# Performance work log

Hardware: AMD Instinct MI355X
Metric: run time of the kernel (lower is better)

The kernel has to match this reference:

```python
import jax, jax.numpy as jnp
import numpy as np

K_NN = 16  # number of nearest neighbors (module init arg k)


def setup_inputs() -> dict:
    key = jax.random.key(0)
    k1, k2 = jax.random.split(key)
    xyz = jax.random.normal(k1, (8, 16384, 3), dtype=jnp.float32)
    centers = jax.random.normal(k2, (8, 1024, 3), dtype=jnp.float32)
    return {"xyz": xyz, "centers": centers}


def reference(xyz, centers):
    # avoiding the (B, N, K, 3) broadcast intermediate of the original while
    # computing the same torch.norm(xyz - centers, dim=-1) math.
    x_sq = jnp.sum(xyz * xyz, axis=-1)          # (B, N)
    c_sq = jnp.sum(centers * centers, axis=-1)  # (B, K)
    cross = jnp.einsum('bnd,bkd->bnk', xyz, centers)  # (B, N, K)
    d2 = x_sq[:, :, None] + c_sq[None if False else slice(None), None, :] - 2.0 * cross
    dist = jnp.sqrt(jnp.maximum(d2, 0.0))       # (B, N, K)
    # torch.topk(dist, k, dim=1, largest=False, sorted=True):
    # smallest-k over the N (points) axis, per center.
    neg = -jnp.transpose(dist, (0, 2, 1))       # (B, K, N)
    _, idx = jax.lax.top_k(neg, K_NN)           # (B, K, k), ascending distance
    return jnp.transpose(idx, (0, 2, 1))        # (B, k, K) to match torch dim=1 topk
```

## Files before the change

kernel.cpp:

```cpp
#include <hip/hip_runtime.h>
#include <stdint.h>

#define BB    8
#define NN    16384
#define KK    1024
#define KNN   16
#define QTR   (NN / 4)
#define QGRP  (QTR / 4)
#define NG64  256
#define GCAP  48
#define SCAP  192

typedef unsigned long long u64;
typedef float f32x2 __attribute__((ext_vector_type(2)));

__device__ __forceinline__ f32x2 pk_fma(f32x2 a, f32x2 b, f32x2 c) {
    f32x2 d;
    asm("v_pk_fma_f32 %0, %1, %2, %3" : "=v"(d) : "v"(a), "v"(b), "v"(c));
    return d;
}
__device__ __forceinline__ f32x2 pk_mul(f32x2 a, f32x2 b) {
    f32x2 d;
    asm("v_pk_mul_f32 %0, %1, %2" : "=v"(d) : "v"(a), "v"(b));
    return d;
}
__device__ __forceinline__ f32x2 pk_add(f32x2 a, f32x2 b) {
    f32x2 d;
    asm("v_pk_add_f32 %0, %1, %2" : "=v"(d) : "v"(a), "v"(b));
    return d;
}
__device__ __forceinline__ float min3f(float a, float b, float c) {
    float d;
    asm("v_min3_f32 %0, %1, %2, %3" : "=v"(d) : "v"(a), "v"(b), "v"(c));
    return d;
}

__device__ __forceinline__ u64 shfl_xor_u64(u64 v, int mask) {
    int lo = (int)(uint32_t)v;
    int hi = (int)(uint32_t)(v >> 32);
    lo = __shfl_xor(lo, mask, 64);
    hi = __shfl_xor(hi, mask, 64);
    return ((u64)(uint32_t)hi << 32) | (u64)(uint32_t)lo;
}

__device__ __forceinline__ u64 shfl_u64(u64 v, int src) {
    int lo = __shfl((int)(uint32_t)v, src, 64);
    int hi = __shfl((int)(uint32_t)(v >> 32), src, 64);
    return ((u64)(uint32_t)hi << 32) | (u64)(uint32_t)lo;
}

__device__ __forceinline__ u64 wave_min_u64(u64 v) {
#pragma unroll
    for (int off = 32; off > 0; off >>= 1) {
        u64 o = shfl_xor_u64(v, off);
        v = o < v ? o : v;
    }
    return v;
}

__device__ __forceinline__ void sort64_kv(u64& key, uint32_t& pay, int lane) {
#pragma unroll
    for (int k = 2; k <= 64; k <<= 1) {
#pragma unroll
        for (int j = k >> 1; j > 0; j >>= 1) {
            u64 okey = shfl_xor_u64(key, j);
            uint32_t opay = (uint32_t)__shfl_xor((int)pay, j, 64);
            bool tmin = ((lane & j) == 0) == ((lane & k) == 0);
            bool osm = okey < key;
            bool take = tmin ? osm : !osm;
            if (take) { key = okey; pay = opay; }
        }
    }
}

__device__ __forceinline__ void sort64_k(u64& key, int lane) {
#pragma unroll
    for (int k = 2; k <= 64; k <<= 1) {
#pragma unroll
        for (int j = k >> 1; j > 0; j >>= 1) {
            u64 okey = shfl_xor_u64(key, j);
            bool tmin = ((lane & j) == 0) == ((lane & k) == 0);
            bool osm = okey < key;
            bool take = tmin ? osm : !osm;
            if (take) key = okey;
        }
    }
}

__device__ __forceinline__ float point_d2(const float* xb, int i,
                                          float c0, float c1, float c2, float csq) {
#pragma clang fp contract(off)
    float x0 = xb[i * 3 + 0];
    float x1 = xb[i * 3 + 1];
    float x2 = xb[i * 3 + 2];
    float xsq = (x0 * x0 + x1 * x1) + x2 * x2;
    float cross = __fmaf_rn(x2, c2, __fmaf_rn(x1, c1, x0 * c0));
    float d2 = (xsq + csq) - 2.0f * cross;
    return d2 < 0.0f ? 0.0f : d2;
}

__device__ __attribute__((noinline)) int fallback_scan(const float* xb,
                                                       float c0, float c1, float c2,
                                                       float csq, int lane) {
    u64 list[KNN];
#pragma unroll
    for (int j = 0; j < KNN; ++j) list[j] = ~0ull;
    for (int i = lane; i < NN; i += 64) {
        float d2 = point_d2(xb, i, c0, c1, c2, csq);
        float dist = __fsqrt_rn(d2);
        u64 key = ((u64)__float_as_uint(dist) << 32) | (u64)(uint32_t)i;
        if (key < list[KNN - 1]) {
#pragma unroll
            for (int j = 0; j < KNN; ++j) {
                bool lt = key < list[j];
                u64 lo = lt ? key : list[j];
                u64 hi = lt ? list[j] : key;
                list[j] = lo;
                key = hi;
            }
        }
    }
    int res = 0;
    for (int it = 0; it < KNN; ++it) {
        u64 best = wave_min_u64(list[0]);
        if (it == lane) res = (int)(uint32_t)best;
        if (list[0] == best) {
#pragma unroll
            for (int j = 0; j < KNN - 1; ++j) list[j] = list[j + 1];
            list[KNN - 1] = ~0ull;
        }
    }
    return res;
}

__device__ __forceinline__ float sixteenth_smallest_f(float v, int lane) {
#pragma unroll
    for (int k = 2; k <= 64; k <<= 1) {
#pragma unroll
        for (int j = k >> 1; j > 0; j >>= 1) {
            float o = __shfl_xor(v, j, 64);
            bool takeMin = ((lane & j) == 0) == ((lane & k) == 0);
            float mn = fminf(v, o);
            float mx = fmaxf(v, o);
            v = takeMin ? mn : mx;
        }
    }
    return __shfl(v, 15, 64);
}

__device__ __forceinline__ void repack_pairs(float4 f0, float4 f1, float4 f2,
                                             f32x2& xl, f32x2& xh,
                                             f32x2& yl, f32x2& yh,
                                             f32x2& zl, f32x2& zh,
                                             f32x2& sl, f32x2& sh) {
    xl = f32x2{f0.x, f0.w};  yl = f32x2{f0.y, f1.x};  zl = f32x2{f0.z, f1.y};
    xh = f32x2{f1.z, f2.y};  yh = f32x2{f1.w, f2.z};  zh = f32x2{f2.x, f2.w};
    sl = pk_add(pk_add(pk_mul(xl, xl), pk_mul(yl, yl)), pk_mul(zl, zl));
    sh = pk_add(pk_add(pk_mul(xh, xh), pk_mul(yh, yh)), pk_mul(zh, zh));
}

__global__ __launch_bounds__(256, 8) void knn_kernel(const float* __restrict__ xyz,
                                                     const float* __restrict__ centers,
                                                     int* __restrict__ out) {
#pragma clang fp contract(off)
    const int q = (int)(threadIdx.x >> 6);
    const int lane = (int)(threadIdx.x & 63);
    const int cbase = (int)blockIdx.x * 4;
    const int b = cbase >> 10;

    __shared__ float    s_min[4][NG64];
    __shared__ uint32_t s_glist[4][GCAP];
    __shared__ uint32_t s_idx[4][SCAP];

    f32x2 nx[4], ny[4], nz[4];
#pragma unroll
    for (int c = 0; c < 4; ++c) {
        float a0 = -2.0f * centers[(cbase + c) * 3 + 0];
        float a1 = -2.0f * centers[(cbase + c) * 3 + 1];
        float a2 = -2.0f * centers[(cbase + c) * 3 + 2];
        nx[c] = f32x2{a0, a0};
        ny[c] = f32x2{a1, a1};
        nz[c] = f32x2{a2, a2};
    }

    const float* xb = xyz + (size_t)b * NN * 3;
    const float4* x4 = (const float4*)xb;
    const int gbase = q * QGRP;

    float acc[4];
#pragma unroll
    for (int c = 0; c < 4; ++c) acc[c] = __builtin_inff();
    {
        const float4* p = x4 + (size_t)(gbase + lane) * 3;
#pragma unroll 4
        for (int s = 0; s < QGRP / 64; ++s, p += 192) {
            float4 f0 = p[0], f1 = p[1], f2 = p[2];
            f32x2 xl, xh, yl, yh, zl, zh, sl, sh;
            repack_pairs(f0, f1, f2, xl, xh, yl, yh, zl, zh, sl, sh);
#pragma unroll
            for (int c = 0; c < 4; ++c) {
                f32x2 dl = pk_fma(xl, nx[c], pk_fma(yl, ny[c], pk_fma(zl, nz[c], sl)));
                f32x2 dh = pk_fma(xh, nx[c], pk_fma(yh, ny[c], pk_fma(zh, nz[c], sh)));
                acc[c] = min3f(acc[c], dl.x, dl.y);
                acc[c] = min3f(acc[c], dh.x, dh.y);
            }
        }
    }
#pragma unroll
    for (int c = 0; c < 4; ++c) s_min[c][threadIdx.x] = acc[c];
    __syncthreads();

    float v = fminf(min3f(s_min[q][lane], s_min[q][64 + lane], s_min[q][128 + lane]),
                    s_min[q][192 + lane]);
    float t16 = sixteenth_smallest_f(v, lane);
    const float Uq = t16 + fabsf(t16) * 1e-5f + 5e-4f;
    const u64 ltmask = (1ull << lane) - 1ull;

    int ng = 0;
#pragma unroll
    for (int it = 0; it < NG64 / 64; ++it) {
        int gi = it * 64 + lane;
        bool cnd = s_min[q][gi] <= Uq;
        u64 m = __ballot(cnd);
        int pos = ng + (int)__popcll(m & ltmask);
        if (cnd && pos < GCAP) s_glist[q][pos] = (uint32_t)gi;
        ng += (int)__popcll(m);
    }
    bool ok = (ng <= GCAP);

    int total = 0;
    if (ok) {
        const int tasks = ng * 16;
        const int trips = (tasks + 63) >> 6;
        for (int t = 0; t < trips; ++t) {
            int j = t * 64 + lane;
            bool valid = j < tasks;
            int grp = (int)s_glist[q][valid ? (j >> 4) : 0];
            int ss = j & 15;
            int lg = (grp >> 6) * QGRP + ss * 64 + (grp & 63);
            float4 f0 = x4[lg * 3 + 0];
            float4 f1 = x4[lg * 3 + 1];
            float4 f2 = x4[lg * 3 + 2];
            f32x2 xl, xh, yl, yh, zl, zh, sl, sh;
            repack_pairs(f0, f1, f2, xl, xh, yl, yh, zl, zh, sl, sh);
            f32x2 dl = pk_fma(xl, nx[q], pk_fma(yl, ny[q], pk_fma(zl, nz[q], sl)));
            f32x2 dh = pk_fma(xh, nx[q], pk_fma(yh, ny[q], pk_fma(zh, nz[q], sh)));
            int ibase = lg * 4;
            bool c0v = valid && (dl.x <= Uq);
            bool c1v = valid && (dl.y <= Uq);
            bool c2v = valid && (dh.x <= Uq);
            bool c3v = valid && (dh.y <= Uq);
            u64 m0 = __ballot(c0v), m1 = __ballot(c1v);
            u64 m2 = __ballot(c2v), m3 = __ballot(c3v);
            int p0 = total + (int)__popcll(m0 & ltmask);
            int b1 = total + (int)__popcll(m0);
            int p1 = b1 + (int)__popcll(m1 & ltmask);
            int b2 = b1 + (int)__popcll(m1);
            int p2 = b2 + (int)__popcll(m2 & ltmask);
            int b3 = b2 + (int)__popcll(m2);
            int p3 = b3 + (int)__popcll(m3 & ltmask);
            if (c0v && p0 < SCAP) s_idx[q][p0] = (uint32_t)(ibase + 0);
            if (c1v && p1 < SCAP) s_idx[q][p1] = (uint32_t)(ibase + 1);
            if (c2v && p2 < SCAP) s_idx[q][p2] = (uint32_t)(ibase + 2);
            if (c3v && p3 < SCAP) s_idx[q][p3] = (uint32_t)(ibase + 3);
            total = b3 + (int)__popcll(m3);
        }
        ok = (total <= SCAP);
    }

    const int cc = cbase + q;
    const float c0 = centers[cc * 3 + 0];
    const float c1 = centers[cc * 3 + 1];
    const float c2 = centers[cc * 3 + 2];
    const float csq = (c0 * c0 + c1 * c1) + c2 * c2;

    uint32_t res;
    if (ok) {
        u64 l0 = ~0ull, l1 = ~0ull, l2 = ~0ull, l3 = ~0ull;
        for (int j = lane; j < total; j += 64) {
            int idx = (int)s_idx[q][j];
            float d2 = point_d2(xb, idx, c0, c1, c2, csq);
            u64 key = ((u64)__float_as_uint(__fsqrt_rn(d2)) << 32) | (u64)(uint32_t)idx;
            bool tt;
            tt = key < l0; { u64 lo = tt ? key : l0, hi = tt ? l0 : key; l0 = lo; key = hi; }
            tt = key < l1; { u64 lo = tt ? key : l1, hi = tt ? l1 : key; l1 = lo; key = hi; }
            tt = key < l2; { u64 lo = tt ? key : l2, hi = tt ? l2 : key; l2 = lo; key = hi; }
            tt = key < l3; { u64 lo = tt ? key : l3, hi = tt ? l3 : key; l3 = lo; key = hi; }
        }
        if (total <= 64) {
            sort64_k(l0, lane);
            res = (uint32_t)l0;
        } else {
            u64 key = l0;
            uint32_t pay = (uint32_t)lane;
            sort64_kv(key, pay, lane);
            int pos = lane >> 2, elem = lane & 3;
            int sid = __shfl((int)pay, pos, 64);
            u64 g0 = shfl_u64(l0, sid);
            u64 g1 = shfl_u64(l1, sid);
            u64 g2 = shfl_u64(l2, sid);
            u64 g3 = shfl_u64(l3, sid);
            u64 gk = (elem == 0) ? g0 : (elem == 1) ? g1 : (elem == 2) ? g2 : g3;
            sort64_k(gk, lane);
            res = (uint32_t)gk;
        }
    } else {
        res = (uint32_t)fallback_scan(xb, c0, c1, c2, csq, lane);
    }

    if (lane < KNN) {
        out[((size_t)b * KNN + lane) * KK + (cc & 1023)] = (int)res;
    }
}

extern "C" void kernel_launch(void* const* d_in, const int* in_sizes, int n_in,
                              void* d_out, int out_size, void* d_ws, size_t ws_size,
                              hipStream_t stream) {
    const float* xyz = (const float*)d_in[0];
    const float* centers = (const float*)d_in[1];
    int* out = (int*)d_out;
    (void)d_ws; (void)ws_size;

    const int nblocks = BB * KK / 4;
    hipLaunchKernelGGL(knn_kernel, dim3(nblocks), dim3(256), 0, stream,
                       xyz, centers, out);
}
```

Measured before the change: 91.16 us.

## Process eight centers per block to reuse each streamed point across more centers

```diff
diff --git a/kernel.cpp b/kernel.cpp
--- a/kernel.cpp
+++ b/kernel.cpp
@@ -5,6 +5,7 @@
 #define NN    16384
 #define KK    1024
 #define KNN   16
+#define CPB   8
 #define QTR   (NN / 4)
 #define QGRP  (QTR / 4)
 #define NG64  256
@@ -159,22 +160,22 @@
     sh = pk_add(pk_add(pk_mul(xh, xh), pk_mul(yh, yh)), pk_mul(zh, zh));
 }
 
-__global__ __launch_bounds__(256, 8) void knn_kernel(const float* __restrict__ xyz,
+__global__ __launch_bounds__(256, 4) void knn_kernel(const float* __restrict__ xyz,
                                                      const float* __restrict__ centers,
                                                      int* __restrict__ out) {
 #pragma clang fp contract(off)
     const int q = (int)(threadIdx.x >> 6);
     const int lane = (int)(threadIdx.x & 63);
-    const int cbase = (int)blockIdx.x * 4;
+    const int cbase = (int)blockIdx.x * CPB;
     const int b = cbase >> 10;
 
-    __shared__ float    s_min[4][NG64];
-    __shared__ uint32_t s_glist[4][GCAP];
-    __shared__ uint32_t s_idx[4][SCAP];
-
-    f32x2 nx[4], ny[4], nz[4];
-#pragma unroll
-    for (int c = 0; c < 4; ++c) {
+    __shared__ float    s_min[CPB][NG64];
+    __shared__ uint32_t s_glist[CPB][GCAP];
+    __shared__ uint32_t s_idx[CPB][SCAP];
+
+    f32x2 nx[CPB], ny[CPB], nz[CPB];
+#pragma unroll
+    for (int c = 0; c < CPB; ++c) {
         float a0 = -2.0f * centers[(cbase + c) * 3 + 0];
         float a1 = -2.0f * centers[(cbase + c) * 3 + 1];
         float a2 = -2.0f * centers[(cbase + c) * 3 + 2];
@@ -187,18 +188,18 @@
     const float4* x4 = (const float4*)xb;
     const int gbase = q * QGRP;
 
-    float acc[4];
-#pragma unroll
-    for (int c = 0; c < 4; ++c) acc[c] = __builtin_inff();
+    float acc[CPB];
+#pragma unroll
+    for (int c = 0; c < CPB; ++c) acc[c] = __builtin_inff();
     {
         const float4* p = x4 + (size_t)(gbase + lane) * 3;
-#pragma unroll 4
+#pragma unroll 2
         for (int s = 0; s < QGRP / 64; ++s, p += 192) {
             float4 f0 = p[0], f1 = p[1], f2 = p[2];
             f32x2 xl, xh, yl, yh, zl, zh, sl, sh;
             repack_pairs(f0, f1, f2, xl, xh, yl, yh, zl, zh, sl, sh);
 #pragma unroll
-            for (int c = 0; c < 4; ++c) {
+            for (int c = 0; c < CPB; ++c) {
                 f32x2 dl = pk_fma(xl, nx[c], pk_fma(yl, ny[c], pk_fma(zl, nz[c], sl)));
                 f32x2 dh = pk_fma(xh, nx[c], pk_fma(yh, ny[c], pk_fma(zh, nz[c], sh)));
                 acc[c] = min3f(acc[c], dl.x, dl.y);
@@ -207,109 +208,119 @@
         }
     }
 #pragma unroll
-    for (int c = 0; c < 4; ++c) s_min[c][threadIdx.x] = acc[c];
+    for (int c = 0; c < CPB; ++c) s_min[c][threadIdx.x] = acc[c];
     __syncthreads();
 
-    float v = fminf(min3f(s_min[q][lane], s_min[q][64 + lane], s_min[q][128 + lane]),
-                    s_min[q][192 + lane]);
-    float t16 = sixteenth_smallest_f(v, lane);
-    const float Uq = t16 + fabsf(t16) * 1e-5f + 5e-4f;
     const u64 ltmask = (1ull << lane) - 1ull;
 
-    int ng = 0;
-#pragma unroll
-    for (int it = 0; it < NG64 / 64; ++it) {
-        int gi = it * 64 + lane;
-        bool cnd = s_min[q][gi] <= Uq;
-        u64 m = __ballot(cnd);
-        int pos = ng + (int)__popcll(m & ltmask);
-        if (cnd && pos < GCAP) s_glist[q][pos] = (uint32_t)gi;
-        ng += (int)__popcll(m);
-    }
-    bool ok = (ng <= GCAP);
-
-    int total = 0;
-    if (ok) {
-        const int tasks = ng * 16;
-        const int trips = (tasks + 63) >> 6;
-        for (int t = 0; t < trips; ++t) {
-            int j = t * 64 + lane;
-            bool valid = j < tasks;
-            int grp = (int)s_glist[q][valid ? (j >> 4) : 0];
-            int ss = j & 15;
-            int lg = (grp >> 6) * QGRP + ss * 64 + (grp & 63);
-            float4 f0 = x4[lg * 3 + 0];
-            float4 f1 = x4[lg * 3 + 1];
-            float4 f2 = x4[lg * 3 + 2];
-            f32x2 xl, xh, yl, yh, zl, zh, sl, sh;
-            repack_pairs(f0, f1, f2, xl, xh, yl, yh, zl, zh, sl, sh);
-            f32x2 dl = pk_fma(xl, nx[q], pk_fma(yl, ny[q], pk_fma(zl, nz[q], sl)));
-            f32x2 dh = pk_fma(xh, nx[q], pk_fma(yh, ny[q], pk_fma(zh, nz[q], sh)));
-            int ibase = lg * 4;
-            bool c0v = valid && (dl.x <= Uq);
-            bool c1v = valid && (dl.y <= Uq);
-            bool c2v = valid && (dh.x <= Uq);
-            bool c3v = valid && (dh.y <= Uq);
-            u64 m0 = __ballot(c0v), m1 = __ballot(c1v);
-            u64 m2 = __ballot(c2v), m3 = __ballot(c3v);
-            int p0 = total + (int)__popcll(m0 & ltmask);
-            int b1 = total + (int)__popcll(m0);
-            int p1 = b1 + (int)__popcll(m1 & ltmask);
-            int b2 = b1 + (int)__popcll(m1);
-            int p2 = b2 + (int)__popcll(m2 & ltmask);
-            int b3 = b2 + (int)__popcll(m2);
-            int p3 = b3 + (int)__popcll(m3 & ltmask);
-            if (c0v && p0 < SCAP) s_idx[q][p0] = (uint32_t)(ibase + 0);
-            if (c1v && p1 < SCAP) s_idx[q][p1] = (uint32_t)(ibase + 1);
-            if (c2v && p2 < SCAP) s_idx[q][p2] = (uint32_t)(ibase + 2);
-            if (c3v && p3 < SCAP) s_idx[q][p3] = (uint32_t)(ibase + 3);
-            total = b3 + (int)__popcll(m3);
-        }
-        ok = (total <= SCAP);
-    }
-
-    const int cc = cbase + q;
-    const float c0 = centers[cc * 3 + 0];
-    const float c1 = centers[cc * 3 + 1];
-    const float c2 = centers[cc * 3 + 2];
-    const float csq = (c0 * c0 + c1 * c1) + c2 * c2;
-
-    uint32_t res;
-    if (ok) {
-        u64 l0 = ~0ull, l1 = ~0ull, l2 = ~0ull, l3 = ~0ull;
-        for (int j = lane; j < total; j += 64) {
-            int idx = (int)s_idx[q][j];
-            float d2 = point_d2(xb, idx, c0, c1, c2, csq);
-            u64 key = ((u64)__float_as_uint(__fsqrt_rn(d2)) << 32) | (u64)(uint32_t)idx;
-            bool tt;
-            tt = key < l0; { u64 lo = tt ? key : l0, hi = tt ? l0 : key; l0 = lo; key = hi; }
-            tt = key < l1; { u64 lo = tt ? key : l1, hi = tt ? l1 : key; l1 = lo; key = hi; }
-            tt = key < l2; { u64 lo = tt ? key : l2, hi = tt ? l2 : key; l2 = lo; key = hi; }
-            tt = key < l3; { u64 lo = tt ? key : l3, hi = tt ? l3 : key; l3 = lo; key = hi; }
-        }
-        if (total <= 64) {
-            sort64_k(l0, lane);
-            res = (uint32_t)l0;
+#pragma unroll
+    for (int ci = 0; ci < 2; ++ci) {
+        const int c = q * 2 + ci;
+        const int cc = cbase + c;
+
+        float v = fminf(min3f(s_min[c][lane], s_min[c][64 + lane],
+                              s_min[c][128 + lane]),
+                        s_min[c][192 + lane]);
+        float t16 = sixteenth_smallest_f(v, lane);
+        const float Uq = t16 + fabsf(t16) * 1e-5f + 5e-4f;
+
+        const float a0 = centers[cc * 3 + 0];
+        const float a1 = centers[cc * 3 + 1];
+        const float a2 = centers[cc * 3 + 2];
+        const f32x2 cnx = f32x2{-2.0f * a0, -2.0f * a0};
+        const f32x2 cny = f32x2{-2.0f * a1, -2.0f * a1};
+        const f32x2 cnz = f32x2{-2.0f * a2, -2.0f * a2};
+
+        int ng = 0;
+#pragma unroll
+        for (int it = 0; it < NG64 / 64; ++it) {
+            int gi = it * 64 + lane;
+            bool cnd = s_min[c][gi] <= Uq;
+            u64 m = __ballot(cnd);
+            int pos = ng + (int)__popcll(m & ltmask);
+            if (cnd && pos < GCAP) s_glist[c][pos] = (uint32_t)gi;
+            ng += (int)__popcll(m);
+        }
+        bool ok = (ng <= GCAP);
+
+        int total = 0;
+        if (ok) {
+            const int tasks = ng * 16;
+            const int trips = (tasks + 63) >> 6;
+            for (int t = 0; t < trips; ++t) {
+                int j = t * 64 + lane;
+                bool valid = j < tasks;
+                int grp = (int)s_glist[c][valid ? (j >> 4) : 0];
+                int ss = j & 15;
+                int lg = (grp >> 6) * QGRP + ss * 64 + (grp & 63);
+                float4 f0 = x4[lg * 3 + 0];
+                float4 f1 = x4[lg * 3 + 1];
+                float4 f2 = x4[lg * 3 + 2];
+                f32x2 xl, xh, yl, yh, zl, zh, sl, sh;
+                repack_pairs(f0, f1, f2, xl, xh, yl, yh, zl, zh, sl, sh);
+                f32x2 dl = pk_fma(xl, cnx, pk_fma(yl, cny, pk_fma(zl, cnz, sl)));
+                f32x2 dh = pk_fma(xh, cnx, pk_fma(yh, cny, pk_fma(zh, cnz, sh)));
+                int ibase = lg * 4;
+                bool c0v = valid && (dl.x <= Uq);
+                bool c1v = valid && (dl.y <= Uq);
+                bool c2v = valid && (dh.x <= Uq);
+                bool c3v = valid && (dh.y <= Uq);
+                u64 m0 = __ballot(c0v), m1 = __ballot(c1v);
+                u64 m2 = __ballot(c2v), m3 = __ballot(c3v);
+                int p0 = total + (int)__popcll(m0 & ltmask);
+                int b1 = total + (int)__popcll(m0);
+                int p1 = b1 + (int)__popcll(m1 & ltmask);
+                int b2 = b1 + (int)__popcll(m1);
+                int p2 = b2 + (int)__popcll(m2 & ltmask);
+                int b3 = b2 + (int)__popcll(m2);
+                int p3 = b3 + (int)__popcll(m3 & ltmask);
+                if (c0v && p0 < SCAP) s_idx[c][p0] = (uint32_t)(ibase + 0);
+                if (c1v && p1 < SCAP) s_idx[c][p1] = (uint32_t)(ibase + 1);
+                if (c2v && p2 < SCAP) s_idx[c][p2] = (uint32_t)(ibase + 2);
+                if (c3v && p3 < SCAP) s_idx[c][p3] = (uint32_t)(ibase + 3);
+                total = b3 + (int)__popcll(m3);
+            }
+            ok = (total <= SCAP);
+        }
+
+        const float csq = (a0 * a0 + a1 * a1) + a2 * a2;
+        uint32_t res;
+        if (ok) {
+            u64 l0 = ~0ull, l1 = ~0ull, l2 = ~0ull, l3 = ~0ull;
+            for (int j = lane; j < total; j += 64) {
+                int idx = (int)s_idx[c][j];
+                float d2 = point_d2(xb, idx, a0, a1, a2, csq);
+                u64 key = ((u64)__float_as_uint(__fsqrt_rn(d2)) << 32) | (u64)(uint32_t)idx;
+                bool tt;
+                tt = key < l0; { u64 lo = tt ? key : l0, hi = tt ? l0 : key; l0 = lo; key = hi; }
+                tt = key < l1; { u64 lo = tt ? key : l1, hi = tt ? l1 : key; l1 = lo; key = hi; }
+                tt = key < l2; { u64 lo = tt ? key : l2, hi = tt ? l2 : key; l2 = lo; key = hi; }
+                tt = key < l3; { u64 lo = tt ? key : l3, hi = tt ? l3 : key; l3 = lo; key = hi; }
+            }
+            if (total <= 64) {
+                sort64_k(l0, lane);
+                res = (uint32_t)l0;
+            } else {
+                u64 key = l0;
+                uint32_t pay = (uint32_t)lane;
+                sort64_kv(key, pay, lane);
+                int pos = lane >> 2, elem = lane & 3;
+                int sid = __shfl((int)pay, pos, 64);
+                u64 g0 = shfl_u64(l0, sid);
+                u64 g1 = shfl_u64(l1, sid);
+                u64 g2 = shfl_u64(l2, sid);
+                u64 g3 = shfl_u64(l3, sid);
+                u64 gk = (elem == 0) ? g0 : (elem == 1) ? g1 : (elem == 2) ? g2 : g3;
+                sort64_k(gk, lane);
+                res = (uint32_t)gk;
+            }
         } else {
-            u64 key = l0;
-            uint32_t pay = (uint32_t)lane;
-            sort64_kv(key, pay, lane);
-            int pos = lane >> 2, elem = lane & 3;
-            int sid = __shfl((int)pay, pos, 64);
-            u64 g0 = shfl_u64(l0, sid);
-            u64 g1 = shfl_u64(l1, sid);
-            u64 g2 = shfl_u64(l2, sid);
-            u64 g3 = shfl_u64(l3, sid);
-            u64 gk = (elem == 0) ? g0 : (elem == 1) ? g1 : (elem == 2) ? g2 : g3;
-            sort64_k(gk, lane);
-            res = (uint32_t)gk;
-        }
-    } else {
-        res = (uint32_t)fallback_scan(xb, c0, c1, c2, csq, lane);
-    }
-
-    if (lane < KNN) {
-        out[((size_t)b * KNN + lane) * KK + (cc & 1023)] = (int)res;
+            res = (uint32_t)fallback_scan(xb, a0, a1, a2, csq, lane);
+        }
+
+        if (lane < KNN) {
+            out[((size_t)b * KNN + lane) * KK + (cc & 1023)] = (int)res;
+        }
     }
 }
 
@@ -321,7 +332,7 @@
     int* out = (int*)d_out;
     (void)d_ws; (void)ws_size;
 
-    const int nblocks = BB * KK / 4;
+    const int nblocks = BB * KK / CPB;
     hipLaunchKernelGGL(knn_kernel, dim3(nblocks), dim3(256), 0, stream,
                        xyz, centers, out);
 }
```

Result: faster. 85.74 us (median of 2 runs) (-5.9%).
